# Optimization experiments

Measured on AMD Instinct MI355X. Metric: run time of the kernel, lower is better.

The kernel has to match this reference:

```python
import jax, jax.numpy as jnp
import numpy as np

H, D = 4, 32  # num_heads, per-head out dim (out_feats=128)
N_AGENT, N_GT, N_UAV = 50000, 50000, 50000
E = 600000
IN = 64


def _gat(x_src, x_dst, src, dst, W_src, W_dst, al, ar, W_res, b, num_dst):
    """DGL-style bipartite GATConv with residual, bias and ReLU activation."""
    fs = (x_src @ W_src).reshape(-1, H, D)      # [Ns,H,D]
    fd = (x_dst @ W_dst).reshape(-1, H, D)      # [Nd,H,D]
    el = jnp.sum(fs * al, axis=-1)              # [Ns,H]
    er = jnp.sum(fd * ar, axis=-1)              # [Nd,H]
    e = jax.nn.leaky_relu(el[src] + er[dst], 0.2)          # [E,H]
    # segment softmax over incoming edges of each dst node
    emax = jax.ops.segment_max(e, dst, num_segments=num_dst)   # [Nd,H], -inf for deg-0
    ee = jnp.exp(e - emax[dst])
    denom = jax.ops.segment_sum(ee, dst, num_segments=num_dst)
    a = ee / denom[dst]                          # [E,H]
    msg = fs[src] * a[:, :, None]                # [E,H,D]
    rst = jax.ops.segment_sum(msg, dst, num_segments=num_dst)  # [Nd,H,D]; zeros for deg-0
    res = (x_dst @ W_res).reshape(-1, H, D)      # residual projection
    out = jax.nn.relu(rst + res + b.reshape(1, H, D))
    return out.reshape(num_dst, H * D)


def setup_inputs() -> dict:
    key = jax.random.key(0)
    ks = jax.random.split(key, 20)
    s = 0.1  # weight init scale
    return {
        'x_gt': jax.random.normal(ks[0], (N_GT, IN), jnp.float32),
        'x_uav': jax.random.normal(ks[1], (N_UAV, IN), jnp.float32),
        'x_agent': jax.random.normal(ks[2], (N_AGENT, IN), jnp.float32),
        'src_gt': jax.random.randint(ks[3], (E,), 0, N_GT, jnp.int32),
        'dst_gt': jax.random.randint(ks[4], (E,), 0, N_AGENT, jnp.int32),
        'src_uav': jax.random.randint(ks[5], (E,), 0, N_UAV, jnp.int32),
        'dst_uav': jax.random.randint(ks[6], (E,), 0, N_AGENT, jnp.int32),
        'W_src_gt': s * jax.random.normal(ks[7], (IN, H * D), jnp.float32),
        'W_dst_gt': s * jax.random.normal(ks[8], (IN, H * D), jnp.float32),
        'attn_l_gt': s * jax.random.normal(ks[9], (H, D), jnp.float32),
        'attn_r_gt': s * jax.random.normal(ks[10], (H, D), jnp.float32),
        'W_res_gt': s * jax.random.normal(ks[11], (IN, H * D), jnp.float32),
        'b_gt': jnp.zeros((H * D,), jnp.float32),
        'W_src_uav': s * jax.random.normal(ks[12], (IN, H * D), jnp.float32),
        'W_dst_uav': s * jax.random.normal(ks[13], (IN, H * D), jnp.float32),
        'attn_l_uav': s * jax.random.normal(ks[14], (H, D), jnp.float32),
        'attn_r_uav': s * jax.random.normal(ks[15], (H, D), jnp.float32),
        'W_res_uav': s * jax.random.normal(ks[16], (IN, H * D), jnp.float32),
        'b_uav': jnp.zeros((H * D,), jnp.float32),
        'W_f': s * jax.random.normal(ks[17], (2 * H * D, H * D), jnp.float32),
        'b_f': jnp.zeros((H * D,), jnp.float32),
    }


def reference(x_gt, x_uav, x_agent, src_gt, dst_gt, src_uav, dst_uav,
              W_src_gt, W_dst_gt, attn_l_gt, attn_r_gt, W_res_gt, b_gt,
              W_src_uav, W_dst_uav, attn_l_uav, attn_r_uav, W_res_uav, b_uav,
              W_f, b_f):
    h_gt = _gat(x_gt, x_agent, src_gt, dst_gt, W_src_gt, W_dst_gt,
                attn_l_gt, attn_r_gt, W_res_gt, b_gt, N_AGENT)
    h_uav = _gat(x_uav, x_agent, src_uav, dst_uav, W_src_uav, W_dst_uav,
                 attn_l_uav, attn_r_uav, W_res_uav, b_uav, N_AGENT)
    h = jnp.concatenate([h_gt, h_uav], axis=1)   # [N_agent, 256]
    return jax.nn.relu(h @ W_f + b_f)            # [N_agent, 128]
```

## Files before the change

### kernel.cpp

```cpp
#include <hip/hip_runtime.h>
#include <hip/hip_bf16.h>

using bf16 = __hip_bfloat16;

#define NA 50000
#define NE 600000

#define NCH 96
#define CHE 12500
#define HROW 100032
#define PBINS 33344

typedef __attribute__((ext_vector_type(8))) short short8;
typedef __attribute__((ext_vector_type(4))) float f32x4;

#define HBUF_B   0u
#define FS_B     25600000u
#define EL_B     51200000u
#define RECS_B   54400000u
#define HIST_B   68800000u
#define ROW_B    78403072u
#define TOPS_B   78803076u
#define FLAG_B   78803588u
#define WST_GT_B 78803600u
#define WST_UAV_B 78819984u
#define WRT_B    78836368u
#define WFT_B    78869136u
#define ELT_GT_B 78934672u
#define ELT_UAV_B 78936720u
#define ERT_B    78938768u
#define WS_BYTES 78940816u

__device__ __forceinline__ float b2f(bf16 v) { return __bfloat162float(v); }

__device__ __forceinline__ float ldf(const void* p, size_t i, int f32) {
    return f32 ? ((const float*)p)[i] : b2f(((const bf16*)p)[i]);
}

__device__ __forceinline__ unsigned short f2bs(float v) {
    bf16 t = __float2bfloat16(v);
    return *(unsigned short*)&t;
}

__device__ __forceinline__ float lrelu_exp(float v) {
    v = v > 0.f ? v : 0.2f * v;
    return __expf(v);
}

__device__ __forceinline__ unsigned int pack_bf16x2(float a, float b) {
    return (unsigned int)f2bs(a) | ((unsigned int)f2bs(b) << 16);
}

__device__ __forceinline__ float lo_f(unsigned int u) { return __uint_as_float(u << 16); }
__device__ __forceinline__ float hi_f(unsigned int u) { return __uint_as_float(u & 0xffff0000u); }

__device__ __forceinline__ short8 ldfrag8(const void* p, size_t off, int f32) {
    if (!f32) return *(const short8*)((const unsigned short*)p + off);
    union { short8 s; unsigned int u[4]; } r;
    const float* fp = (const float*)p + off;
#pragma unroll
    for (int j = 0; j < 4; ++j) r.u[j] = pack_bf16x2(fp[2 * j], fp[2 * j + 1]);
    return r.s;
}

__device__ int probe_f32(const void* x0) {
    __shared__ int cnt;
    if (threadIdx.x == 0) cnt = 0;
    __syncthreads();
    const bf16* p = (const bf16*)x0;
    int bad = 0;
    for (int i = threadIdx.x; i < 1024; i += 256) {
        float av = fabsf(b2f(p[i]));
        if (!(av <= 1e6f)) bad++;
    }
    if (bad) atomicAdd(&cnt, bad);
    __syncthreads();
    return cnt > 8;
}

__global__ void HeteroVisionConv_29703993819529_kernel(
    const void* x0,
    const void* Wsg, const void* alg, const void* Wdg, const void* arg_,
    const void* Wsu, const void* alu, const void* Wdu, const void* aru,
    const void* Wrg, const void* Wru, const void* Wf,
    unsigned short* wsT_gt, unsigned short* wsT_uav, unsigned short* wrT,
    unsigned short* wfT, unsigned short* elT_gt, unsigned short* elT_uav,
    unsigned short* erT,
    int* flag, unsigned int* outp, long sent) {
    int b = blockIdx.x, t = threadIdx.x;
    int f32 = probe_f32(x0);
    if (b == 20) {
        if (t == 0) { flag[0] = f32; outp[sent] = 0x447A447Au; }
        return;
    }
    if (b < 8) {
        for (int i = t; i < 16 * 256; i += 256) {
            int n = b * 16 + (i >> 8), k = i & 255;
            wfT[n * 256 + k] = f2bs(ldf(Wf, (size_t)k * 128 + n, f32));
        }
    } else if (b < 12) {
        for (int i = t; i < 64 * 64; i += 256) {
            int n = (b - 8) * 64 + (i >> 6), k = i & 63;
            float v = (n < 128) ? ldf(Wrg, (size_t)k * 128 + n, f32)
                                : ldf(Wru, (size_t)k * 128 + (n - 128), f32);
            wrT[n * 64 + k] = f2bs(v);
        }
    } else if (b < 14) {
        for (int i = t; i < 64 * 64; i += 256) {
            int n = (b - 12) * 64 + (i >> 6), k = i & 63;
            wsT_gt[n * 64 + k] = f2bs(ldf(Wsg, (size_t)k * 128 + n, f32));
        }
    } else if (b < 16) {
        for (int i = t; i < 64 * 64; i += 256) {
            int n = (b - 14) * 64 + (i >> 6), k = i & 63;
            wsT_uav[n * 64 + k] = f2bs(ldf(Wsu, (size_t)k * 128 + n, f32));
        }
    } else {
        int m = b - 16;
        const void* Wm = (m == 0) ? Wsg : (m == 1) ? Wdg : (m == 2) ? Wsu : Wdu;
        const void* Am = (m == 0) ? alg : (m == 1) ? arg_ : (m == 2) ? alu : aru;
        int k = t >> 2, h = t & 3;
        float a = 0.f;
        for (int d = 0; d < 32; ++d)
            a += ldf(Wm, (size_t)k * 128 + h * 32 + d, f32) *
                 ldf(Am, (size_t)h * 32 + d, f32);
        unsigned short v = f2bs(a);
        if (m == 0) {
            elT_gt[h * 64 + k] = v;
            for (int i = t; i < 12 * 64; i += 256) elT_gt[(4 + (i >> 6)) * 64 + (i & 63)] = 0;
        } else if (m == 2) {
            elT_uav[h * 64 + k] = v;
            for (int i = t; i < 12 * 64; i += 256) elT_uav[(4 + (i >> 6)) * 64 + (i & 63)] = 0;
        } else if (m == 1) {
            erT[h * 64 + k] = v;
        } else {
            erT[(4 + h) * 64 + k] = v;
            for (int i = t; i < 8 * 64; i += 256) erT[(8 + (i >> 6)) * 64 + (i & 63)] = 0;
        }
    }
}

__global__ void fused_k(const int* dg, const int* du,
                        unsigned char* hist,
                        const void* xg, const void* xu, const void* xa,
                        const unsigned short* wsT_gt, const unsigned short* wsT_uav,
                        const unsigned short* elT_gt, const unsigned short* elT_uav,
                        const unsigned short* wrT, const unsigned short* erT,
                        const void* bg, const void* bu,
                        float* elbase, bf16* fs, bf16* hbuf, const int* flag) {
    __shared__ unsigned short Bt[256 * 72];
    __shared__ float bl[256];
    int b = blockIdx.x, t = threadIdx.x;

    if (b < NCH) {
        int c = b;
        int g = c >= 48;
        const int* dp = (g ? du : dg) + (c - g * 48) * CHE;
        unsigned int* h32 = (unsigned int*)Bt;
        for (int p = 0; p < 3; ++p) {
            int binLo = p * PBINS;
            unsigned int* out = (unsigned int*)(hist + (size_t)c * HROW + binLo);
            bool live = (binLo + PBINS > g * NA) && (binLo < g * NA + NA);
            if (!live) {
                for (int i = t; i < PBINS / 4; i += 256) out[i] = 0u;
                continue;
            }
            for (int i = t; i < PBINS / 4; i += 256) h32[i] = 0u;
            __syncthreads();
            for (int i = t; i < CHE / 4; i += 256) {
                int4 d4 = *(const int4*)(dp + i * 4);
                int dd[4] = {d4.x, d4.y, d4.z, d4.w};
#pragma unroll
                for (int k = 0; k < 4; ++k) {
                    int rel = g * NA + dd[k] - binLo;
                    if (rel >= 0 && rel < PBINS)
                        atomicAdd(&h32[rel >> 2], 1u << (8 * (rel & 3)));
                }
            }
            __syncthreads();
            for (int i = t; i < PBINS / 4; i += 256) out[i] = h32[i];
            __syncthreads();
        }
        return;
    }
    int nidx = b - NCH;
    int f32 = *flag;
    int lane = t & 63, w = t >> 6;
    int m = lane & 15, quad = lane >> 4;

    if (nidx < 1564) {
        int g = nidx / 782, bb = nidx % 782;
        const void* A = g ? xu : xg;
        const unsigned short* WT = g ? wsT_uav : wsT_gt;
        const unsigned short* ET = g ? elT_uav : elT_gt;
        float* elout = elbase + (g ? 400000 : 0);
        bf16* out = fs + (size_t)g * NA * 128;
        for (int i = t * 8; i < 128 * 64; i += 256 * 8) {
            short8 v = *(const short8*)(WT + i);
            int n = i >> 6, k = i & 63;
            *(short8*)&Bt[n * 72 + k] = v;
        }
        __syncthreads();
        int row = bb * 64 + w * 16 + m;
        int rowc = row < NA ? row : NA - 1;
        short8 a0 = ldfrag8(A, (size_t)rowc * 64 + quad * 8, f32);
        short8 a1 = ldfrag8(A, (size_t)rowc * 64 + 32 + quad * 8, f32);
        f32x4 acc[8];
#pragma unroll
        for (int nt = 0; nt < 8; ++nt) acc[nt] = (f32x4){0.f, 0.f, 0.f, 0.f};
#pragma unroll
        for (int nt = 0; nt < 8; ++nt) {
            short8 b0 = *(const short8*)&Bt[(nt * 16 + m) * 72 + quad * 8];
            short8 b1 = *(const short8*)&Bt[(nt * 16 + m) * 72 + 32 + quad * 8];
            acc[nt] = __builtin_amdgcn_mfma_f32_16x16x32_bf16(a0, b0, acc[nt], 0, 0, 0);
            acc[nt] = __builtin_amdgcn_mfma_f32_16x16x32_bf16(a1, b1, acc[nt], 0, 0, 0);
        }
        f32x4 eacc = (f32x4){0.f, 0.f, 0.f, 0.f};
        {
            short8 e0 = *(const short8*)&ET[m * 64 + quad * 8];
            short8 e1 = *(const short8*)&ET[m * 64 + 32 + quad * 8];
            eacc = __builtin_amdgcn_mfma_f32_16x16x32_bf16(a0, e0, eacc, 0, 0, 0);
            eacc = __builtin_amdgcn_mfma_f32_16x16x32_bf16(a1, e1, eacc, 0, 0, 0);
        }
        int srow = bb * 64 + w * 16 + quad * 4;
#pragma unroll
        for (int nt = 0; nt < 8; ++nt) {
#pragma unroll
            for (int r = 0; r < 4; ++r) {
                int rr = srow + r;
                if (rr < NA) out[(size_t)rr * 128 + nt * 16 + m] = __float2bfloat16(acc[nt][r]);
            }
        }
        if (m < 4) {
#pragma unroll
            for (int r = 0; r < 4; ++r) {
                int rr = srow + r;
                if (rr < NA) elout[(size_t)rr * 4 + m] = eacc[r];
            }
        }
        return;
    }
    int bb = nidx - 1564;
    for (int i = t * 8; i < 256 * 64; i += 256 * 8) {
        short8 v = *(const short8*)(wrT + i);
        int n = i >> 6, k = i & 63;
        *(short8*)&Bt[n * 72 + k] = v;
    }
    bl[t] = (t < 128) ? ldf(bg, t, f32) : ldf(bu, t - 128, f32);
    __syncthreads();
    int row = bb * 64 + w * 16 + m;
    int rowc = row < NA ? row : NA - 1;
    short8 a0 = ldfrag8(xa, (size_t)rowc * 64 + quad * 8, f32);
    short8 a1 = ldfrag8(xa, (size_t)rowc * 64 + 32 + quad * 8, f32);
    f32x4 acc[16];
#pragma unroll
    for (int nt = 0; nt < 16; ++nt) acc[nt] = (f32x4){0.f, 0.f, 0.f, 0.f};
#pragma unroll
    for (int nt = 0; nt < 16; ++nt) {
        short8 b0 = *(const short8*)&Bt[(nt * 16 + m) * 72 + quad * 8];
        short8 b1 = *(const short8*)&Bt[(nt * 16 + m) * 72 + 32 + quad * 8];
        acc[nt] = __builtin_amdgcn_mfma_f32_16x16x32_bf16(a0, b0, acc[nt], 0, 0, 0);
        acc[nt] = __builtin_amdgcn_mfma_f32_16x16x32_bf16(a1, b1, acc[nt], 0, 0, 0);
    }
    f32x4 eacc = (f32x4){0.f, 0.f, 0.f, 0.f};
    {
        short8 e0 = *(const short8*)&erT[m * 64 + quad * 8];
        short8 e1 = *(const short8*)&erT[m * 64 + 32 + quad * 8];
        eacc = __builtin_amdgcn_mfma_f32_16x16x32_bf16(a0, e0, eacc, 0, 0, 0);
        eacc = __builtin_amdgcn_mfma_f32_16x16x32_bf16(a1, e1, eacc, 0, 0, 0);
    }
    int srow = bb * 64 + w * 16 + quad * 4;
#pragma unroll
    for (int nt = 0; nt < 16; ++nt) {
        int col = nt * 16 + m;
#pragma unroll
        for (int r = 0; r < 4; ++r) {
            int rr = srow + r;
            if (rr < NA)
                hbuf[(size_t)rr * 256 + col] = __float2bfloat16(acc[nt][r] + bl[col]);
        }
    }
    if (m < 8) {
        float* ero = (m < 4) ? (elbase + 200000) : (elbase + 600000);
        int mm = m & 3;
#pragma unroll
        for (int r = 0; r < 4; ++r) {
            int rr = srow + r;
            if (rr < NA) ero[(size_t)rr * 4 + mm] = eacc[r];
        }
    }
}

__global__ void scan1_k(unsigned char* hist, unsigned int* row, unsigned int* tops) {
    __shared__ unsigned char ch[NCH * 1024];
    __shared__ unsigned int sh[256];
    int b = blockIdx.x, t = threadIdx.x;
    int base = b * 1024;
    int off = base + t * 4;
    for (int c = 0; c < NCH; ++c) {
        unsigned int w = 0u;
        if (off + 4 <= HROW) w = *(const unsigned int*)(hist + (size_t)c * HROW + off);
        *(unsigned int*)&ch[c * 1024 + t * 4] = w;
    }
    __syncthreads();
    unsigned int v[4];
    for (int j = 0; j < 4; ++j) {
        int idx = t * 4 + j;
        unsigned int run = 0;
        for (int c = 0; c < NCH; ++c) {
            unsigned int x = ch[c * 1024 + idx];
            ch[c * 1024 + idx] = (unsigned char)run;
            run += x;
        }
        v[j] = (base + idx < 100000) ? run : 0u;
    }
    __syncthreads();
    for (int c = 0; c < NCH; ++c) {
        if (off + 4 <= HROW)
            *(unsigned int*)(hist + (size_t)c * HROW + off) =
                *(const unsigned int*)&ch[c * 1024 + t * 4];
    }
    unsigned int s = v[0] + v[1] + v[2] + v[3];
    sh[t] = s;
    __syncthreads();
    for (int o = 1; o < 256; o <<= 1) {
        unsigned int x = (t >= o) ? sh[t - o] : 0u;
        __syncthreads();
        sh[t] += x;
        __syncthreads();
    }
    unsigned int run = sh[t] - s;
    for (int j = 0; j < 4; ++j) {
        if (base + j + t * 4 < 100000) row[base + t * 4 + j] = run;
        run += v[j];
    }
    if (t == 255) tops[b] = sh[255];
}

__global__ void scan2_k(unsigned int* tops, unsigned int* row) {
    __shared__ unsigned int sh[128];
    int t = threadIdx.x;
    unsigned int v = (t < 98) ? tops[t] : 0u;
    sh[t] = v;
    __syncthreads();
    for (int off = 1; off < 128; off <<= 1) {
        unsigned int x = (t >= off) ? sh[t - off] : 0u;
        __syncthreads();
        sh[t] += x;
        __syncthreads();
    }
    if (t < 98) tops[t] = sh[t] - v;
    if (t == 97) row[100000] = sh[97];
}

__global__ void scan3_k(unsigned int* row, const unsigned int* tops) {
    int b = blockIdx.x, t = threadIdx.x;
    unsigned int off = tops[b];
    for (int i = b * 1024 + t; i < b * 1024 + 1024; i += 256) {
        if (i < 100000) row[i] += off;
    }
}

__global__ void rank_scatter_k(const int* sg, const int* dg, const int* su, const int* du,
                               const float* elbase, const unsigned int* row,
                               const unsigned char* hist, unsigned int* recs) {
    __shared__ unsigned int h32[6252];
    int b = blockIdx.x, t = threadIdx.x;
    int c = b >> 2, q = b & 3;
    int binLo = q * 25008;
    for (int i = t; i < 6252; i += 256) h32[i] = 0u;
    __syncthreads();
    int g = c >= 48;
    int eoff = (c - g * 48) * CHE;
    const int* sp = (g ? su : sg) + eoff;
    const int* dp = (g ? du : dg) + eoff;
    const float4* el4 = (const float4*)(elbase + (g ? 400000 : 0));
    const float4* er4 = (const float4*)(elbase + (g ? 600000 : 200000));
    const unsigned char* cb = hist + (size_t)c * HROW;
    for (int i = t; i < CHE / 4; i += 256) {
        int4 s4 = *(const int4*)(sp + i * 4);
        int4 d4 = *(const int4*)(dp + i * 4);
        int ss[4] = {s4.x, s4.y, s4.z, s4.w};
        int dd[4] = {d4.x, d4.y, d4.z, d4.w};
#pragma unroll
        for (int k = 0; k < 4; ++k) {
            int bin = g * NA + dd[k];
            int rel = bin - binLo;
            if (rel < 0 || rel >= 25008) continue;
            unsigned int sh8 = 8u * (rel & 3);
            unsigned int old = atomicAdd(&h32[rel >> 2], 1u << sh8);
            unsigned int lr = (old >> sh8) & 255u;
            unsigned int pos = row[bin] + (unsigned int)cb[bin] + lr;
            float4 l = el4[ss[k]], r = er4[dd[k]];
            uint3 rec;
            rec.x = (unsigned int)ss[k];
            rec.y = pack_bf16x2(lrelu_exp(l.x + r.x), lrelu_exp(l.y + r.y));
            rec.z = pack_bf16x2(lrelu_exp(l.z + r.z), lrelu_exp(l.w + r.w));
            *(uint3*)(recs + (size_t)pos * 3) = rec;
        }
    }
}

__global__ void gather_k(const unsigned int* row, const unsigned int* recs,
                         const bf16* fs, bf16* hbuf) {
    int wid = (blockIdx.x * 256 + threadIdx.x) >> 6;
    int lane = threadIdx.x & 63;
    if (wid >= 2 * NA) return;
    int g = wid / NA, d = wid - g * NA;
    int eg = lane >> 4;
    int cl = lane & 15;
    int hsel = cl >> 3;
    int hodd = (cl >> 2) & 1;
    unsigned int start = row[g * NA + d];
    unsigned int end   = row[g * NA + d + 1];
    const uint4* fs4 = (const uint4*)(fs + (size_t)g * NA * 128);

    float denom = 0.f;
    float a[8];
#pragma unroll
    for (int k = 0; k < 8; ++k) a[k] = 0.f;

    if (start < end) {
        uint3 rr[4], rn[4];
#pragma unroll
        for (int j = 0; j < 4; ++j) {
            unsigned int idx = start + 4 * j + eg;
            rr[j] = *(const uint3*)(recs + (size_t)(idx < end ? idx : end - 1) * 3);
        }
        for (unsigned int i = start; i < end; i += 16) {
            uint4 uu[4];
#pragma unroll
            for (int j = 0; j < 4; ++j) uu[j] = fs4[(size_t)rr[j].x * 16 + cl];
            unsigned int inext = i + 16;
#pragma unroll
            for (int j = 0; j < 4; ++j) {
                unsigned int idx = inext + 4 * j + eg;
                rn[j] = *(const uint3*)(recs + (size_t)(idx < end ? idx : end - 1) * 3);
            }
#pragma unroll
            for (int j = 0; j < 4; ++j) {
                unsigned int idx = i + 4 * j + eg;
                unsigned int pp = hsel ? rr[j].z : rr[j].y;
                float e = hodd ? hi_f(pp) : lo_f(pp);
                if (idx >= end) e = 0.f;
                denom += e;
                a[0] += lo_f(uu[j].x) * e;
                a[1] += hi_f(uu[j].x) * e;
                a[2] += lo_f(uu[j].y) * e;
                a[3] += hi_f(uu[j].y) * e;
                a[4] += lo_f(uu[j].z) * e;
                a[5] += hi_f(uu[j].z) * e;
                a[6] += lo_f(uu[j].w) * e;
                a[7] += hi_f(uu[j].w) * e;
            }
#pragma unroll
            for (int j = 0; j < 4; ++j) rr[j] = rn[j];
        }
    }
#pragma unroll
    for (int k = 0; k < 8; ++k) {
        a[k] += __shfl_xor(a[k], 16, 64);
        a[k] += __shfl_xor(a[k], 32, 64);
    }
    denom += __shfl_xor(denom, 16, 64);
    denom += __shfl_xor(denom, 32, 64);
    if (lane < 16) {
        float inv = (end > start) ? 1.f / denom : 0.f;
        uint4* hp = (uint4*)(hbuf + (size_t)d * 256 + g * 128) + cl;
        uint4 rv = *hp;
        float v0 = a[0] * inv + lo_f(rv.x);
        float v1 = a[1] * inv + hi_f(rv.x);
        float v2 = a[2] * inv + lo_f(rv.y);
        float v3 = a[3] * inv + hi_f(rv.y);
        float v4 = a[4] * inv + lo_f(rv.z);
        float v5 = a[5] * inv + hi_f(rv.z);
        float v6 = a[6] * inv + lo_f(rv.w);
        float v7 = a[7] * inv + hi_f(rv.w);
        v0 = v0 > 0.f ? v0 : 0.f;
        v1 = v1 > 0.f ? v1 : 0.f;
        v2 = v2 > 0.f ? v2 : 0.f;
        v3 = v3 > 0.f ? v3 : 0.f;
        v4 = v4 > 0.f ? v4 : 0.f;
        v5 = v5 > 0.f ? v5 : 0.f;
        v6 = v6 > 0.f ? v6 : 0.f;
        v7 = v7 > 0.f ? v7 : 0.f;
        uint4 o;
        o.x = pack_bf16x2(v0, v1);
        o.y = pack_bf16x2(v2, v3);
        o.z = pack_bf16x2(v4, v5);
        o.w = pack_bf16x2(v6, v7);
        *hp = o;
    }
}

__global__ void final_k(const bf16* hbuf, const unsigned short* wfT,
                        const void* bfp, void* outp, const int* flag) {
    int f32 = *flag;
    int b = blockIdx.x;
    __shared__ unsigned short Bt[128 * 72];
    __shared__ float bl[128];
    int t = threadIdx.x;
    if (t < 128) bl[t] = ldf(bfp, t, f32);
    int lane = t & 63, w = t >> 6;
    int m = lane & 15, quad = lane >> 4;
    int row = b * 64 + w * 16 + m;
    int rowc = row < NA ? row : NA - 1;
    f32x4 acc[8];
#pragma unroll
    for (int nt = 0; nt < 8; ++nt) acc[nt] = (f32x4){0.f, 0.f, 0.f, 0.f};
    for (int kc = 0; kc < 4; ++kc) {
        __syncthreads();
        for (int i = t * 8; i < 128 * 64; i += 256 * 8) {
            int n = i >> 6, k = i & 63;
            short8 v = *(const short8*)(wfT + (size_t)n * 256 + kc * 64 + k);
            *(short8*)&Bt[n * 72 + k] = v;
        }
        __syncthreads();
        short8 a0 = *(const short8*)((const unsigned short*)hbuf +
                                     (size_t)rowc * 256 + kc * 64 + quad * 8);
        short8 a1 = *(const short8*)((const unsigned short*)hbuf +
                                     (size_t)rowc * 256 + kc * 64 + 32 + quad * 8);
#pragma unroll
        for (int nt = 0; nt < 8; ++nt) {
            short8 b0 = *(const short8*)&Bt[(nt * 16 + m) * 72 + quad * 8];
            short8 b1 = *(const short8*)&Bt[(nt * 16 + m) * 72 + 32 + quad * 8];
            acc[nt] = __builtin_amdgcn_mfma_f32_16x16x32_bf16(a0, b0, acc[nt], 0, 0, 0);
            acc[nt] = __builtin_amdgcn_mfma_f32_16x16x32_bf16(a1, b1, acc[nt], 0, 0, 0);
        }
    }
    int srow = b * 64 + w * 16 + quad * 4;
#pragma unroll
    for (int nt = 0; nt < 8; ++nt) {
        int col = nt * 16 + m;
        float bv = bl[col];
#pragma unroll
        for (int r = 0; r < 4; ++r) {
            int rr = srow + r;
            if (rr < NA) {
                float v = acc[nt][r] + bv;
                v = v > 0.f ? v : 0.f;
                if (f32) ((float*)outp)[(size_t)rr * 128 + col] = v;
                else ((bf16*)outp)[(size_t)rr * 128 + col] = __float2bfloat16(v);
            }
        }
    }
}

extern "C" void kernel_launch(void* const* d_in, const int* in_sizes, int n_in,
                              void* d_out, int out_size, void* d_ws, size_t ws_size,
                              hipStream_t stream) {
    const void* x_gt     = d_in[0];
    const void* x_uav    = d_in[1];
    const void* x_ag     = d_in[2];
    const int*  src_gt   = (const int*)d_in[3];
    const int*  dst_gt   = (const int*)d_in[4];
    const int*  src_uav  = (const int*)d_in[5];
    const int*  dst_uav  = (const int*)d_in[6];
    const void* Wsrc_gt  = d_in[7];
    const void* Wdst_gt  = d_in[8];
    const void* al_gt    = d_in[9];
    const void* ar_gt    = d_in[10];
    const void* Wres_gt  = d_in[11];
    const void* b_gt     = d_in[12];
    const void* Wsrc_uav = d_in[13];
    const void* Wdst_uav = d_in[14];
    const void* al_uav   = d_in[15];
    const void* ar_uav   = d_in[16];
    const void* Wres_uav = d_in[17];
    const void* b_uav    = d_in[18];
    const void* W_f      = d_in[19];
    const void* b_f      = d_in[20];

    char* wsb = (char*)d_ws;
    bf16* hbuf = (bf16*)(wsb + HBUF_B);
    bf16* fs = (bf16*)(wsb + FS_B);
    float* el = (float*)(wsb + EL_B);
    unsigned int* recs = (unsigned int*)(wsb + RECS_B);
    unsigned char* hist = (unsigned char*)(wsb + HIST_B);
    unsigned int* row = (unsigned int*)(wsb + ROW_B);
    unsigned int* tops = (unsigned int*)(wsb + TOPS_B);
    int* flag = (int*)(wsb + FLAG_B);
    unsigned short* wsT_gt = (unsigned short*)(wsb + WST_GT_B);
    unsigned short* wsT_uav = (unsigned short*)(wsb + WST_UAV_B);
    unsigned short* wrT = (unsigned short*)(wsb + WRT_B);
    unsigned short* wfT = (unsigned short*)(wsb + WFT_B);
    unsigned short* elT_gt = (unsigned short*)(wsb + ELT_GT_B);
    unsigned short* elT_uav = (unsigned short*)(wsb + ELT_UAV_B);
    unsigned short* erT = (unsigned short*)(wsb + ERT_B);

    if (ws_size < (size_t)WS_BYTES) {
        hipMemsetAsync(d_out, 0x42, (size_t)out_size * 2, stream);
        return;
    }

    long sent = (long)out_size / 2 - 1;

    HeteroVisionConv_29703993819529_kernel<<<21, 256, 0, stream>>>(
        x_gt, Wsrc_gt, al_gt, Wdst_gt, ar_gt, Wsrc_uav, al_uav, Wdst_uav, ar_uav,
        Wres_gt, Wres_uav, W_f,
        wsT_gt, wsT_uav, wrT, wfT, elT_gt, elT_uav, erT,
        flag, (unsigned int*)d_out, sent);
    fused_k<<<NCH + 2346, 256, 0, stream>>>(dst_gt, dst_uav, hist,
                                            x_gt, x_uav, x_ag,
                                            wsT_gt, wsT_uav, elT_gt, elT_uav,
                                            wrT, erT, b_gt, b_uav,
                                            el, fs, hbuf, flag);
    scan1_k<<<98, 256, 0, stream>>>(hist, row, tops);
    scan2_k<<<1, 128, 0, stream>>>(tops, row);
    scan3_k<<<98, 256, 0, stream>>>(row, tops);
    rank_scatter_k<<<NCH * 4, 256, 0, stream>>>(src_gt, dst_gt, src_uav, dst_uav,
                                                el, row, hist, recs);
    gather_k<<<25000, 256, 0, stream>>>(row, recs, fs, hbuf);
    final_k<<<782, 256, 0, stream>>>(hbuf, wfT, b_f, d_out, flag);
}
```

Measured before the change: 310.5 us.

## Record per-edge local rank during histogram, make scatter a flat per-edge kernel

The histogram phase of fused_k now stores each edge's intra-chunk rank (the old value returned by the LDS atomic) into a new byte array. The scatter kernel then needs no LDS histogram rebuild: one thread per edge reads rank, chunk offset and row start and writes its record. This removes the second round of shared-memory atomics and the 4x redundant edge scans across bin quarters in rank_scatter. In exchange it adds a 1.2 MB rank buffer with byte-sized writes and reads, plus uncoalesced per-edge hist lookups.

```diff
diff --git a/kernel.cpp b/kernel.cpp
--- a/kernel.cpp
+++ b/kernel.cpp
@@ -29,7 +29,8 @@
 #define ELT_GT_B 78934672u
 #define ELT_UAV_B 78936720u
 #define ERT_B    78938768u
-#define WS_BYTES 78940816u
+#define RANK8_B  78940816u
+#define WS_BYTES 80140816u
 
 __device__ __forceinline__ float b2f(bf16 v) { return __bfloat162float(v); }
 
@@ -141,7 +142,7 @@
 }
 
 __global__ void fused_k(const int* dg, const int* du,
-                        unsigned char* hist,
+                        unsigned char* hist, unsigned char* rank8,
                         const void* xg, const void* xu, const void* xa,
                         const unsigned short* wsT_gt, const unsigned short* wsT_uav,
                         const unsigned short* elT_gt, const unsigned short* elT_uav,
@@ -155,7 +156,9 @@
     if (b < NCH) {
         int c = b;
         int g = c >= 48;
-        const int* dp = (g ? du : dg) + (c - g * 48) * CHE;
+        int eoff = (c - g * 48) * CHE;
+        const int* dp = (g ? du : dg) + eoff;
+        unsigned char* rk = rank8 + (size_t)g * NE + eoff;
         unsigned int* h32 = (unsigned int*)Bt;
         for (int p = 0; p < 3; ++p) {
             int binLo = p * PBINS;
@@ -173,8 +176,11 @@
 #pragma unroll
                 for (int k = 0; k < 4; ++k) {
                     int rel = g * NA + dd[k] - binLo;
-                    if (rel >= 0 && rel < PBINS)
-                        atomicAdd(&h32[rel >> 2], 1u << (8 * (rel & 3)));
+                    if (rel >= 0 && rel < PBINS) {
+                        unsigned int sh8 = 8u * (rel & 3);
+                        unsigned int old = atomicAdd(&h32[rel >> 2], 1u << sh8);
+                        rk[i * 4 + k] = (unsigned char)((old >> sh8) & 255u);
+                    }
                 }
             }
             __syncthreads();
@@ -361,44 +367,29 @@
     }
 }
 
-__global__ void rank_scatter_k(const int* sg, const int* dg, const int* su, const int* du,
-                               const float* elbase, const unsigned int* row,
-                               const unsigned char* hist, unsigned int* recs) {
-    __shared__ unsigned int h32[6252];
-    int b = blockIdx.x, t = threadIdx.x;
-    int c = b >> 2, q = b & 3;
-    int binLo = q * 25008;
-    for (int i = t; i < 6252; i += 256) h32[i] = 0u;
-    __syncthreads();
-    int g = c >= 48;
-    int eoff = (c - g * 48) * CHE;
-    const int* sp = (g ? su : sg) + eoff;
-    const int* dp = (g ? du : dg) + eoff;
+__global__ void scatter_k(const int* sg, const int* dg, const int* su, const int* du,
+                          const float* elbase, const unsigned int* row,
+                          const unsigned char* hist, const unsigned char* rank8,
+                          unsigned int* recs) {
+    int idx = blockIdx.x * 256 + threadIdx.x;
+    if (idx >= 2 * NE) return;
+    int g = idx >= NE;
+    int e = idx - g * NE;
+    int s = (g ? su : sg)[e];
+    int d = (g ? du : dg)[e];
+    int c = g * 48 + e / CHE;
+    int bin = g * NA + d;
     const float4* el4 = (const float4*)(elbase + (g ? 400000 : 0));
     const float4* er4 = (const float4*)(elbase + (g ? 600000 : 200000));
-    const unsigned char* cb = hist + (size_t)c * HROW;
-    for (int i = t; i < CHE / 4; i += 256) {
-        int4 s4 = *(const int4*)(sp + i * 4);
-        int4 d4 = *(const int4*)(dp + i * 4);
-        int ss[4] = {s4.x, s4.y, s4.z, s4.w};
-        int dd[4] = {d4.x, d4.y, d4.z, d4.w};
-#pragma unroll
-        for (int k = 0; k < 4; ++k) {
-            int bin = g * NA + dd[k];
-            int rel = bin - binLo;
-            if (rel < 0 || rel >= 25008) continue;
-            unsigned int sh8 = 8u * (rel & 3);
-            unsigned int old = atomicAdd(&h32[rel >> 2], 1u << sh8);
-            unsigned int lr = (old >> sh8) & 255u;
-            unsigned int pos = row[bin] + (unsigned int)cb[bin] + lr;
-            float4 l = el4[ss[k]], r = er4[dd[k]];
-            uint3 rec;
-            rec.x = (unsigned int)ss[k];
-            rec.y = pack_bf16x2(lrelu_exp(l.x + r.x), lrelu_exp(l.y + r.y));
-            rec.z = pack_bf16x2(lrelu_exp(l.z + r.z), lrelu_exp(l.w + r.w));
-            *(uint3*)(recs + (size_t)pos * 3) = rec;
-        }
-    }
+    unsigned int lr = rank8[idx];
+    unsigned int cb = hist[(size_t)c * HROW + bin];
+    unsigned int pos = row[bin] + cb + lr;
+    float4 l = el4[s], r = er4[d];
+    uint3 rec;
+    rec.x = (unsigned int)s;
+    rec.y = pack_bf16x2(lrelu_exp(l.x + r.x), lrelu_exp(l.y + r.y));
+    rec.z = pack_bf16x2(lrelu_exp(l.z + r.z), lrelu_exp(l.w + r.w));
+    *(uint3*)(recs + (size_t)pos * 3) = rec;
 }
 
 __global__ void gather_k(const unsigned int* row, const unsigned int* recs,
@@ -587,6 +578,7 @@
     unsigned short* elT_gt = (unsigned short*)(wsb + ELT_GT_B);
     unsigned short* elT_uav = (unsigned short*)(wsb + ELT_UAV_B);
     unsigned short* erT = (unsigned short*)(wsb + ERT_B);
+    unsigned char* rank8 = (unsigned char*)(wsb + RANK8_B);
 
     if (ws_size < (size_t)WS_BYTES) {
         hipMemsetAsync(d_out, 0x42, (size_t)out_size * 2, stream);
@@ -600,7 +592,7 @@
         Wres_gt, Wres_uav, W_f,
         wsT_gt, wsT_uav, wrT, wfT, elT_gt, elT_uav, erT,
         flag, (unsigned int*)d_out, sent);
-    fused_k<<<NCH + 2346, 256, 0, stream>>>(dst_gt, dst_uav, hist,
+    fused_k<<<NCH + 2346, 256, 0, stream>>>(dst_gt, dst_uav, hist, rank8,
                                             x_gt, x_uav, x_ag,
                                             wsT_gt, wsT_uav, elT_gt, elT_uav,
                                             wrT, erT, b_gt, b_uav,
@@ -608,8 +600,8 @@
     scan1_k<<<98, 256, 0, stream>>>(hist, row, tops);
     scan2_k<<<1, 128, 0, stream>>>(tops, row);
     scan3_k<<<98, 256, 0, stream>>>(row, tops);
-    rank_scatter_k<<<NCH * 4, 256, 0, stream>>>(src_gt, dst_gt, src_uav, dst_uav,
-                                                el, row, hist, recs);
+    scatter_k<<<4688, 256, 0, stream>>>(src_gt, dst_gt, src_uav, dst_uav,
+                                        el, row, hist, rank8, recs);
     gather_k<<<25000, 256, 0, stream>>>(row, recs, fs, hbuf);
     final_k<<<782, 256, 0, stream>>>(hbuf, wfT, b_f, d_out, flag);
 }
```

New measurement: 302.2 us. -2.7%, faster.
